# Optimization experiments

Measured on AMD Instinct MI355X. Metric: run time of the kernel, lower is better.

## Reference

```python
import jax, jax.numpy as jnp
import numpy as np

LEAK = 0.2
NUM_GRAPHS = 64


def _gat(h_in, src, dst, eh, W, att_src, att_dst, att_edge, lin_edge_W, bias, N):
    # PyG GATConv with edge_dim, concat=False (mean over heads)
    H, C = att_src.shape
    h = (h_in @ W).reshape(N, H, C)                      # [N,H,C]
    e = (eh @ lin_edge_W).reshape(-1, H, C)              # [Eaug,H,C]
    a_s = jnp.einsum('nhc,hc->nh', h, att_src)           # [N,H]
    a_d = jnp.einsum('nhc,hc->nh', h, att_dst)
    a_e = jnp.einsum('ehc,hc->eh', e, att_edge)          # [Eaug,H]
    score = jax.nn.leaky_relu(a_s[src] + a_d[dst] + a_e, LEAK)
    # scatter-softmax over incoming edges of each destination node
    m = jax.ops.segment_max(score, dst, num_segments=N)
    ex = jnp.exp(score - m[dst])
    den = jax.ops.segment_sum(ex, dst, num_segments=N)
    alpha = ex / den[dst]                                # [Eaug,H]
    out = jax.ops.segment_sum(alpha[:, :, None] * h[src], dst, num_segments=N)
    return out.mean(axis=1) + bias                       # concat=False -> head mean


def setup_inputs() -> dict:
    key = jax.random.key(0)
    ks = jax.random.split(key, 32)
    N, E, F, FE, HID, H, NT = 30000, 480000, 64, 16, 64, 4, 16
    Cin1 = F + HID
    s = 0.05
    d = {
        'x': jax.random.normal(ks[0], (N, F), jnp.float32),
        'edge_attr': jax.random.normal(ks[1], (E, FE), jnp.float32),
        'node_emb': jax.random.normal(ks[2], (NT, HID), jnp.float32) * s,
        'edge_W': jax.random.normal(ks[3], (FE, HID), jnp.float32) * s,
        'edge_b': jnp.zeros((HID,), jnp.float32),
        'W1': jax.random.normal(ks[4], (Cin1, H * HID), jnp.float32) * s,
        'as1': jax.random.normal(ks[5], (H, HID), jnp.float32) * s,
        'ad1': jax.random.normal(ks[6], (H, HID), jnp.float32) * s,
        'ae1': jax.random.normal(ks[7], (H, HID), jnp.float32) * s,
        'leW1': jax.random.normal(ks[8], (HID, H * HID), jnp.float32) * s,
        'b1': jnp.zeros((HID,), jnp.float32),
        'W2': jax.random.normal(ks[9], (HID, H * HID), jnp.float32) * s,
        'as2': jax.random.normal(ks[10], (H, HID), jnp.float32) * s,
        'ad2': jax.random.normal(ks[11], (H, HID), jnp.float32) * s,
        'ae2': jax.random.normal(ks[12], (H, HID), jnp.float32) * s,
        'leW2': jax.random.normal(ks[13], (HID, H * HID), jnp.float32) * s,
        'b2': jnp.zeros((HID,), jnp.float32),
        'sage_Wl': jax.random.normal(ks[14], (HID, HID), jnp.float32) * s,
        'sage_bl': jnp.zeros((HID,), jnp.float32),
        'sage_Wr': jax.random.normal(ks[15], (HID, HID), jnp.float32) * s,
        'lin1_W': jax.random.normal(ks[16], (HID, HID), jnp.float32) * s,
        'lin1_b': jnp.zeros((HID,), jnp.float32),
        'lin2_W': jax.random.normal(ks[17], (HID, HID), jnp.float32) * s,
        'lin2_b': jnp.zeros((HID,), jnp.float32),
        'tel_W': jax.random.normal(ks[18], (HID, 1), jnp.float32) * s,
        'tel_b': jnp.zeros((1,), jnp.float32),
        'comp_W': jax.random.normal(ks[19], (HID, 1), jnp.float32) * s,
        'comp_b': jnp.zeros((1,), jnp.float32),
        'pch_W': jax.random.normal(ks[20], (HID, 1), jnp.float32) * s,
        'pch_b': jnp.zeros((1,), jnp.float32),
        'edge_index': jax.random.randint(ks[21], (2, E), 0, N, jnp.int32),
        'batch': jnp.sort(jax.random.randint(ks[22], (N,), 0, NUM_GRAPHS, jnp.int32)),
        'node_type': jax.random.randint(ks[23], (N,), 0, NT, jnp.int32),
    }
    return d


def reference(x, edge_attr, node_emb, edge_W, edge_b,
              W1, as1, ad1, ae1, leW1, b1,
              W2, as2, ad2, ae2, leW2, b2,
              sage_Wl, sage_bl, sage_Wr,
              lin1_W, lin1_b, lin2_W, lin2_b,
              tel_W, tel_b, comp_W, comp_b, pch_W, pch_b,
              edge_index, batch, node_type):
    N = x.shape[0]
    src0, dst0 = edge_index[0], edge_index[1]

    h0 = jnp.concatenate([x, node_emb[node_type]], axis=-1)   # [N, F+HID]
    eh = edge_attr @ edge_W + edge_b                          # [E, HID]

    # GATConv default add_self_loops=True, fill_value='mean' on edge_attr
    loop = jnp.arange(N, dtype=src0.dtype)
    src = jnp.concatenate([src0, loop])
    dst = jnp.concatenate([dst0, loop])
    eh_aug = jnp.concatenate([eh, jnp.broadcast_to(eh.mean(axis=0), (N, eh.shape[1]))], axis=0)

    h1 = jax.nn.elu(_gat(h0, src, dst, eh_aug, W1, as1, ad1, ae1, leW1, b1, N))
    h2 = jax.nn.elu(_gat(h1, src, dst, eh_aug, W2, as2, ad2, ae2, leW2, b2, N))

    # SAGEConv: mean neighbor aggregation (src->dst) + root transform
    deg = jax.ops.segment_sum(jnp.ones_like(dst0, dtype=h2.dtype), dst0, num_segments=N)
    agg = jax.ops.segment_sum(h2[src0], dst0, num_segments=N) / jnp.clip(deg, 1.0)[:, None]
    h3 = jax.nn.elu(agg @ sage_Wl + sage_bl + h2 @ sage_Wr)

    # global mean pool per graph
    cnt = jax.ops.segment_sum(jnp.ones((N,), h3.dtype), batch, num_segments=NUM_GRAPHS)
    g = jax.ops.segment_sum(h3, batch, num_segments=NUM_GRAPHS) / jnp.clip(cnt, 1.0)[:, None]

    g = jax.nn.elu(g @ lin1_W + lin1_b)                       # dropout inactive (eval)
    g = g @ lin2_W + lin2_b
    return (g @ tel_W + tel_b, g @ comp_W + comp_b, g @ pch_W + pch_b)
```

## Files before the change

kernel.cpp:

```cpp
#include <hip/hip_runtime.h>
#include <hip/hip_fp16.h>
#include <math.h>

#define NN 30000
#define NE 480000
#define FEA 16
#define HID 64
#define NG 64
#define LEAKK 0.2f

#define S_AEL1   0
#define S_AEL2   4
#define S_KF1    16
#define S_C1     80
#define S_KF2    88
#define S_C2     152
#define S_MS1    160
#define S_MD1    672
#define S_MS2    1184
#define S_MD2    1440
#define S_EAS    1700

#define BT1H 0
#define BT1L 20480
#define BT2H 40960
#define BT2L 57344
#define BT3H 73728
#define BT3L 81920

typedef __attribute__((ext_vector_type(8))) short short8;
typedef __attribute__((ext_vector_type(4))) float f32x4;

__device__ __forceinline__ float eluf(float v) { return v > 0.f ? v : expm1f(v); }
__device__ __forceinline__ float leakyf(float v) { return v >= 0.f ? v : LEAKK * v; }
__device__ __forceinline__ void fma4(float4& a, float w, const float4& x) {
    a.x += w * x.x; a.y += w * x.y; a.z += w * x.z; a.w += w * x.w;
}
__device__ __forceinline__ unsigned bf16pack(float a, float b) {
    unsigned ua = __float_as_uint(a), ub = __float_as_uint(b);
    ua = (ua + 0x7FFFu + ((ua >> 16) & 1u)) >> 16;
    ub = (ub + 0x7FFFu + ((ub >> 16) & 1u)) >> 16;
    return ua | (ub << 16);
}
__device__ __forceinline__ unsigned short bf1(float v) {
    unsigned u = __float_as_uint(v);
    return (unsigned short)((u + 0x7FFFu + ((u >> 16) & 1u)) >> 16);
}
__device__ __forceinline__ float bf1tof(unsigned short h) {
    return __uint_as_float(((unsigned)h) << 16);
}
__device__ __forceinline__ uint2 bfpack4(float a, float b, float c, float d) {
    return make_uint2(bf16pack(a, b), bf16pack(c, d));
}
__device__ __forceinline__ float4 bf16x4(uint2 p) {
    float4 r;
    r.x = __uint_as_float(p.x << 16);
    r.y = __uint_as_float(p.x & 0xFFFF0000u);
    r.z = __uint_as_float(p.y << 16);
    r.w = __uint_as_float(p.y & 0xFFFF0000u);
    return r;
}
__device__ __forceinline__ unsigned h2pack(float a, float b) {
    __half2 h = __floats2half2_rn(a, b);
    return *(unsigned*)&h;
}
__device__ __forceinline__ float2 h2unpack(unsigned u) {
    __half2 h = *(__half2*)&u;
    return __half22float2(h);
}
__device__ __forceinline__ float4 h4tof(uint2 p) {
    float2 lo = h2unpack(p.x), hi = h2unpack(p.y);
    return make_float4(lo.x, lo.y, hi.x, hi.y);
}
__device__ __forceinline__ float4 escore4(float4 a, float4 b, float4 c) {
    float4 r;
    r.x = expf(leakyf(a.x + b.x + c.x));
    r.y = expf(leakyf(a.y + b.y + c.y));
    r.z = expf(leakyf(a.z + b.z + c.z));
    r.w = expf(leakyf(a.w + b.w + c.w));
    return r;
}


__global__ __launch_bounds__(256) void cm_prepw_kernel(
    const int* __restrict__ dst, const float* __restrict__ EA,
    int* __restrict__ cnt, int* __restrict__ rank,
    const float* __restrict__ W1, const float* __restrict__ W2,
    const float* __restrict__ Wl, const float* __restrict__ Wr,
    const float* __restrict__ emb,
    const float* __restrict__ leW1, const float* __restrict__ aew1,
    const float* __restrict__ leW2, const float* __restrict__ aew2,
    const float* __restrict__ edge_W, const float* __restrict__ edge_b,
    const float* __restrict__ as1, const float* __restrict__ ad1,
    const float* __restrict__ as2, const float* __restrict__ ad2,
    const int* __restrict__ batch,
    unsigned short* __restrict__ BT,
    float* __restrict__ S, int* __restrict__ goff) {
    int t = threadIdx.x, bx = blockIdx.x;
    if (bx < 176) {
        int i = bx * 256 + t;
        float v = 0.f;
        int dsti = -1;
        if (i < 16384) {
            int kk = i >> 6, c = i & 63;
            int h = kk >> 6, k = kk & 63;
            v = 0.25f * W1[k * 256 + h * 64 + c];
            dsti = BT1H + c * 320 + kk;
        } else if (i < 20480) {
            int j2 = i - 16384;
            int r2 = j2 >> 6, c = j2 & 63;
            int tau = r2 >> 2, h = r2 & 3;
            float acc = 0.f;
            for (int j = 0; j < 64; j++)
                acc += emb[tau * 64 + j] * W1[(64 + j) * 256 + h * 64 + c];
            v = 0.25f * acc;
            dsti = BT1H + c * 320 + 256 + r2;
        } else if (i < 36864) {
            int j = i - 20480;
            int kk = j >> 6, c = j & 63;
            int h = kk >> 6, k = kk & 63;
            v = 0.25f * W2[k * 256 + h * 64 + c];
            dsti = BT2H + c * 256 + kk;
        } else if (i < 45056) {
            int j = i - 36864;
            int k = j >> 6, c = j & 63;
            v = (k < 64) ? Wl[k * 64 + c] : Wr[(k - 64) * 64 + c];
            dsti = BT3H + c * 128 + k;
        }
        if (dsti >= 0) {
            unsigned short hi = bf1(v);
            unsigned short lo = bf1(v - bf1tof(hi));
            BT[dsti] = hi;
            BT[dsti + 20480 - ((dsti >= BT2H) ? ((dsti >= BT3H) ? 12288 : 4096) : 0)] = lo;
        }
        return;
    }
    if (bx < 178) {
        int i = (bx - 176) * 256 + t;
        int k = i >> 2, h = i & 3;
        float s = 0.f, d = 0.f;
        for (int c = 0; c < 64; c++) {
            float w = W1[k * 256 + h * 64 + c];
            s += w * as1[h * 64 + c];
            d += w * ad1[h * 64 + c];
        }
        S[S_MS1 + i] = s; S[S_MD1 + i] = d;
        return;
    }
    if (bx == 178) {
        int k = t >> 2, h = t & 3;
        float s = 0.f, d = 0.f;
        for (int c = 0; c < 64; c++) {
            float w = W2[k * 256 + h * 64 + c];
            s += w * as2[h * 64 + c];
            d += w * ad2[h * 64 + c];
        }
        S[S_MS2 + t] = s; S[S_MD2 + t] = d;
        return;
    }
    if (bx == 179) {
        __shared__ float M1s[256], M2s[256];
        {
            int k = t >> 2, h = t & 3;
            float m1 = 0.f, m2 = 0.f;
            for (int c = 0; c < 64; c++) {
                m1 += leW1[k * 256 + h * 64 + c] * aew1[h * 64 + c];
                m2 += leW2[k * 256 + h * 64 + c] * aew2[h * 64 + c];
            }
            M1s[t] = m1; M2s[t] = m2;
        }
        __syncthreads();
        if (t < 64) {
            int f = t >> 2, h = t & 3;
            float k1 = 0.f, k2 = 0.f;
            for (int k = 0; k < 64; k++) {
                k1 += edge_W[f * 64 + k] * M1s[k * 4 + h];
                k2 += edge_W[f * 64 + k] * M2s[k * 4 + h];
            }
            S[S_KF1 + t] = k1; S[S_KF2 + t] = k2;
        } else if (t < 68) {
            int h = t - 64;
            float c1 = 0.f, c2 = 0.f;
            for (int k = 0; k < 64; k++) {
                c1 += edge_b[k] * M1s[k * 4 + h];
                c2 += edge_b[k] * M2s[k * 4 + h];
            }
            S[S_C1 + h] = c1; S[S_C2 + h] = c2;
        }
        return;
    }
    if (bx == 180) {
        if (t > NG) return;
        int lo = 0, hi = NN;
        while (lo < hi) {
            int mid = (lo + hi) >> 1;
            if (batch[mid] < t) lo = mid + 1; else hi = mid;
        }
        goff[t] = lo;
        return;
    }
    if (bx < 245) {
        __shared__ float4 red4[16];
        int cb = bx - 181;
        int c4 = (t & 3) * 4;
        int r0 = cb * 64 + (t >> 2);
        float4 a0 = {0, 0, 0, 0}, a1 = a0, a2 = a0, a3 = a0;
        for (int r = r0; r < NE; r += 16384) {
            int r1 = r + 4096, r2 = r + 8192, r3 = r + 12288;
            float4 v0 = *(const float4*)(EA + (size_t)r * FEA + c4);
            float4 v1 = (r1 < NE) ? *(const float4*)(EA + (size_t)r1 * FEA + c4)
                                  : make_float4(0, 0, 0, 0);
            float4 v2 = (r2 < NE) ? *(const float4*)(EA + (size_t)r2 * FEA + c4)
                                  : make_float4(0, 0, 0, 0);
            float4 v3 = (r3 < NE) ? *(const float4*)(EA + (size_t)r3 * FEA + c4)
                                  : make_float4(0, 0, 0, 0);
            a0.x += v0.x; a0.y += v0.y; a0.z += v0.z; a0.w += v0.w;
            a1.x += v1.x; a1.y += v1.y; a1.z += v1.z; a1.w += v1.w;
            a2.x += v2.x; a2.y += v2.y; a2.z += v2.z; a2.w += v2.w;
            a3.x += v3.x; a3.y += v3.y; a3.z += v3.z; a3.w += v3.w;
        }
        float4 acc;
        acc.x = (a0.x + a1.x) + (a2.x + a3.x);
        acc.y = (a0.y + a1.y) + (a2.y + a3.y);
        acc.z = (a0.z + a1.z) + (a2.z + a3.z);
        acc.w = (a0.w + a1.w) + (a2.w + a3.w);
#pragma unroll
        for (int mask = 4; mask < 64; mask <<= 1) {
            acc.x += __shfl_xor(acc.x, mask, 64);
            acc.y += __shfl_xor(acc.y, mask, 64);
            acc.z += __shfl_xor(acc.z, mask, 64);
            acc.w += __shfl_xor(acc.w, mask, 64);
        }
        int lane = t & 63, wid = t >> 6;
        if (lane < 4) red4[wid * 4 + lane] = acc;
        __syncthreads();
        if (t < 4) {
            float4 a = red4[t], b = red4[4 + t], c = red4[8 + t], d = red4[12 + t];
            atomicAdd(&S[S_EAS + t * 4 + 0], a.x + b.x + c.x + d.x);
            atomicAdd(&S[S_EAS + t * 4 + 1], a.y + b.y + c.y + d.y);
            atomicAdd(&S[S_EAS + t * 4 + 2], a.z + b.z + c.z + d.z);
            atomicAdd(&S[S_EAS + t * 4 + 3], a.w + b.w + c.w + d.w);
        }
        return;
    }
    int e = (bx - 245) * 256 + t;
    if (e < NE) rank[e] = atomicAdd(&cnt[dst[e]], 1);
}

__global__ void scan_blocks_kernel(const int* __restrict__ cnt, int* __restrict__ eoff,
                                   int* __restrict__ bsum) {
    __shared__ int wsum[16];
    int t = threadIdx.x;
    int i = blockIdx.x * 1024 + t;
    int v = (i < NN) ? cnt[i] : 0;
    int lane = t & 63;
    int incl = v;
#pragma unroll
    for (int ofs = 1; ofs < 64; ofs <<= 1) {
        int u = __shfl_up(incl, ofs, 64);
        if (lane >= ofs) incl += u;
    }
    int wid = t >> 6;
    if (lane == 63) wsum[wid] = incl;
    __syncthreads();
    if (t < 16) {
        int s = wsum[t];
#pragma unroll
        for (int ofs = 1; ofs < 16; ofs <<= 1) {
            int u = __shfl_up(s, ofs, 64);
            if (t >= ofs) s += u;
        }
        wsum[t] = s;
    }
    __syncthreads();
    int excl = incl - v + (wid > 0 ? wsum[wid - 1] : 0);
    if (i < NN) eoff[i] = excl;
    if (t == 1023) bsum[blockIdx.x] = excl + v;
}

__global__ __launch_bounds__(256) void scanadd_attn_kernel(
    const int* __restrict__ bsum, int* __restrict__ eoff,
    const float* __restrict__ x, const float* __restrict__ node_emb,
    const int* __restrict__ node_type, float* __restrict__ S,
    float* __restrict__ as_, float* __restrict__ ad_, unsigned* __restrict__ xb) {
    __shared__ float xt[64 * 132];
    __shared__ float ms[512], md[512];
    __shared__ int ntS[64];
    int t = threadIdx.x;
    if (blockIdx.x < 118) {
        int j = blockIdx.x >> 2;
        int pref = 0;
        for (int u = 0; u < j; u++) pref += bsum[u];
        int i = blockIdx.x * 256 + t;
        if (i < NN) eoff[i] += pref;
        if (i == 0) eoff[NN] = NE;
        return;
    }
    if (blockIdx.x == 118) {
        if (t < 8) {
            int h = t & 3;
            const float* KF = (t < 4) ? (S + S_KF1) : (S + S_KF2);
            const float* C  = (t < 4) ? (S + S_C1)  : (S + S_C2);
            float acc = (float)NE * C[h];
            for (int f = 0; f < 16; f++) acc += S[S_EAS + f] * KF[f * 4 + h];
            S[((t < 4) ? S_AEL1 : S_AEL2) + h] = acc;
        }
        return;
    }
    int n0 = (blockIdx.x - 119) * 64;
    if (t < 64) {
        int n = n0 + t;
        ntS[t] = (n < NN) ? node_type[n] : 0;
    }
    for (int i = t; i < 512; i += 256) { ms[i] = S[S_MS1 + i]; md[i] = S[S_MD1 + i]; }
    __syncthreads();
    for (int i = t; i < 1024; i += 256) {
        int r = i >> 4, c4 = (i & 15) * 4;
        int n = n0 + r;
        float4 f = {0, 0, 0, 0};
        if (n < NN) f = *(const float4*)(x + (size_t)n * 64 + c4);
        *(float4*)&xt[r * 132 + c4] = f;
    }
    for (int i = t; i < 1024; i += 256) {
        int r = i >> 4, c4 = (i & 15) * 4;
        int n = n0 + r;
        float4 f = {0, 0, 0, 0};
        if (n < NN) f = *(const float4*)(node_emb + (size_t)ntS[r] * 64 + c4);
        *(float4*)&xt[r * 132 + 64 + c4] = f;
    }
    __syncthreads();
    for (int i = t; i < 2048; i += 256) {
        int r = i >> 5, u = i & 31;
        int n = n0 + r;
        if (n < NN)
            xb[(size_t)n * 32 + u] = bf16pack(xt[r * 132 + 2 * u], xt[r * 132 + 2 * u + 1]);
    }
    int r = t >> 2, h = t & 3;
    float s = 0.f, d = 0.f;
#pragma unroll 8
    for (int k = 0; k < 128; k++) {
        float xv = xt[r * 132 + k];
        s += xv * ms[k * 4 + h];
        d += xv * md[k * 4 + h];
    }
    int n = n0 + r;
    if (n < NN) { as_[n * 4 + h] = s; ad_[n * 4 + h] = d; }
}

__global__ __launch_bounds__(256) void scatter_proj_kernel(
    const int* __restrict__ src, const int* __restrict__ dst,
    const float* __restrict__ EA, const float* __restrict__ S,
    const float* __restrict__ as_, const float* __restrict__ ad_,
    const int* __restrict__ node_type,
    const int* __restrict__ eoff, const int* __restrict__ rank,
    uint4* __restrict__ recs) {
    __shared__ float KF1s[64], KF2s[64], Cs[8];
    int t = threadIdx.x;
    if (t < 64) { KF1s[t] = S[S_KF1 + t]; KF2s[t] = S[S_KF2 + t]; }
    else if (t < 72) { int q = t - 64; Cs[q] = (q < 4) ? S[S_C1 + q] : S[S_C2 + q - 4]; }
    __syncthreads();
    int e0 = blockIdx.x * 512 + t;
#pragma unroll
    for (int u = 0; u < 2; u++) {
        int e = e0 + u * 256;
        if (e < NE) {
            int s = src[e], d = dst[e];
            float a1[4], a2[4];
#pragma unroll
            for (int h = 0; h < 4; h++) { a1[h] = Cs[h]; a2[h] = Cs[4 + h]; }
            const float4* EA4 = (const float4*)(EA + (size_t)e * FEA);
#pragma unroll
            for (int q = 0; q < 4; q++) {
                float4 v = EA4[q];
                float vv[4] = {v.x, v.y, v.z, v.w};
#pragma unroll
                for (int j = 0; j < 4; j++) {
                    int f = q * 4 + j;
#pragma unroll
                    for (int h = 0; h < 4; h++) {
                        a1[h] += vv[j] * KF1s[f * 4 + h];
                        a2[h] += vv[j] * KF2s[f * 4 + h];
                    }
                }
            }
            int pos = eoff[d] + rank[e];
            float4 asv = ((const float4*)as_)[s];
            float4 adv = ((const float4*)ad_)[d];
            float4 w1 = escore4(asv, adv, make_float4(a1[0], a1[1], a1[2], a1[3]));
            uint4 lo = make_uint4(h2pack(w1.x, w1.y), h2pack(w1.z, w1.w),
                                  h2pack(a2[0], a2[1]), h2pack(a2[2], a2[3]));
            uint4 hi = make_uint4((unsigned)(s | (node_type[s] << 16)), (unsigned)d, 0u, 0u);
            recs[2 * pos] = lo;
            recs[2 * pos + 1] = hi;
        }
    }
}

__global__ __launch_bounds__(256) void score2_kernel(
    uint4* __restrict__ recs,
    const float* __restrict__ as_, const float* __restrict__ ad_,
    int* __restrict__ sepc) {
    int p = blockIdx.x * 256 + threadIdx.x;
    uint2 a2h = ((const uint2*)recs)[4 * p + 1];
    int2 sd = ((const int2*)recs)[4 * p + 2];
    int s = sd.x & 0xFFFF;
    float4 w2 = escore4(((const float4*)as_)[s], ((const float4*)ad_)[sd.y], h4tof(a2h));
    ((uint2*)recs)[4 * p + 1] = make_uint2(h2pack(w2.x, w2.y), h2pack(w2.z, w2.w));
    sepc[p] = sd.x;
}

__global__ __launch_bounds__(256) void agg_gat1_kernel(
    const int* __restrict__ eoff, const uint4* __restrict__ recs,
    const unsigned* __restrict__ xb,
    const int* __restrict__ node_type,
    const float* __restrict__ as_, const float* __restrict__ ad_,
    const float* __restrict__ S, uint2* __restrict__ aggb) {
    int n = blockIdx.x * 4 + (threadIdx.x >> 6);
    if (n >= NN) return;
    int lane = threadIdx.x & 63;
    int sub = lane >> 4, ch = lane & 15;
    const uint2* Xb = (const uint2*)xb;
    const int* RI = (const int*)recs;
    const uint2* RW = (const uint2*)recs;
    float4 asn = ((const float4*)as_)[n];
    float4 adn = ((const float4*)ad_)[n];
    float4 a0 = {0, 0, 0, 0}, a1 = a0, a2 = a0, a3 = a0, dn = a0, tw = a0;
    int b = eoff[n], e_end = eoff[n + 1];
    int nE = e_end - b;
    int i = sub;
    for (; i + 4 < nE; i += 8) {
        int p0 = b + i, p1 = p0 + 4;
        int q0 = RI[8 * p0 + 4], q1 = RI[8 * p1 + 4];
        int s0 = q0 & 0xFFFF, t0 = q0 >> 16;
        int s1 = q1 & 0xFFFF, t1 = q1 >> 16;
        float4 w0 = h4tof(RW[4 * p0]), w1 = h4tof(RW[4 * p1]);
        float4 x0 = bf16x4(Xb[(size_t)s0 * 16 + ch]);
        float4 x1 = bf16x4(Xb[(size_t)s1 * 16 + ch]);
        fma4(a0, w0.x, x0); fma4(a1, w0.y, x0); fma4(a2, w0.z, x0); fma4(a3, w0.w, x0);
        fma4(a0, w1.x, x1); fma4(a1, w1.y, x1); fma4(a2, w1.z, x1); fma4(a3, w1.w, x1);
        dn.x += w0.x + w1.x; dn.y += w0.y + w1.y;
        dn.z += w0.z + w1.z; dn.w += w0.w + w1.w;
        if (ch == t0) { tw.x += w0.x; tw.y += w0.y; tw.z += w0.z; tw.w += w0.w; }
        if (ch == t1) { tw.x += w1.x; tw.y += w1.y; tw.z += w1.z; tw.w += w1.w; }
    }
    for (; i < nE; i += 4) {
        int p0 = b + i;
        int q0 = RI[8 * p0 + 4];
        int s0 = q0 & 0xFFFF, t0 = q0 >> 16;
        float4 w0 = h4tof(RW[4 * p0]);
        float4 x0 = bf16x4(Xb[(size_t)s0 * 16 + ch]);
        fma4(a0, w0.x, x0); fma4(a1, w0.y, x0); fma4(a2, w0.z, x0); fma4(a3, w0.w, x0);
        dn.x += w0.x; dn.y += w0.y; dn.z += w0.z; dn.w += w0.w;
        if (ch == t0) { tw.x += w0.x; tw.y += w0.y; tw.z += w0.z; tw.w += w0.w; }
    }
    if (sub == 0) {
        const float inv = 1.f / (float)NE;
        float e0 = expf(leakyf(asn.x + adn.x + S[S_AEL1 + 0] * inv));
        float e1 = expf(leakyf(asn.y + adn.y + S[S_AEL1 + 1] * inv));
        float e2 = expf(leakyf(asn.z + adn.z + S[S_AEL1 + 2] * inv));
        float e3 = expf(leakyf(asn.w + adn.w + S[S_AEL1 + 3] * inv));
        float4 xs = bf16x4(Xb[(size_t)n * 16 + ch]);
        fma4(a0, e0, xs); fma4(a1, e1, xs); fma4(a2, e2, xs); fma4(a3, e3, xs);
        dn.x += e0; dn.y += e1; dn.z += e2; dn.w += e3;
        int tn = node_type[n];
        if (ch == tn) { tw.x += e0; tw.y += e1; tw.z += e2; tw.w += e3; }
    }
#pragma unroll
    for (int mask = 16; mask < 64; mask <<= 1) {
        a0.x += __shfl_xor(a0.x, mask, 64); a0.y += __shfl_xor(a0.y, mask, 64);
        a0.z += __shfl_xor(a0.z, mask, 64); a0.w += __shfl_xor(a0.w, mask, 64);
        a1.x += __shfl_xor(a1.x, mask, 64); a1.y += __shfl_xor(a1.y, mask, 64);
        a1.z += __shfl_xor(a1.z, mask, 64); a1.w += __shfl_xor(a1.w, mask, 64);
        a2.x += __shfl_xor(a2.x, mask, 64); a2.y += __shfl_xor(a2.y, mask, 64);
        a2.z += __shfl_xor(a2.z, mask, 64); a2.w += __shfl_xor(a2.w, mask, 64);
        a3.x += __shfl_xor(a3.x, mask, 64); a3.y += __shfl_xor(a3.y, mask, 64);
        a3.z += __shfl_xor(a3.z, mask, 64); a3.w += __shfl_xor(a3.w, mask, 64);
        dn.x += __shfl_xor(dn.x, mask, 64); dn.y += __shfl_xor(dn.y, mask, 64);
        dn.z += __shfl_xor(dn.z, mask, 64); dn.w += __shfl_xor(dn.w, mask, 64);
        tw.x += __shfl_xor(tw.x, mask, 64); tw.y += __shfl_xor(tw.y, mask, 64);
        tw.z += __shfl_xor(tw.z, mask, 64); tw.w += __shfl_xor(tw.w, mask, 64);
    }
    if (sub == 0) {
        float i0 = 1.f / dn.x, i1 = 1.f / dn.y, i2 = 1.f / dn.z, i3 = 1.f / dn.w;
        uint2* A2 = aggb + (size_t)n * 80;
        A2[ch]      = bfpack4(a0.x * i0, a0.y * i0, a0.z * i0, a0.w * i0);
        A2[16 + ch] = bfpack4(a1.x * i1, a1.y * i1, a1.z * i1, a1.w * i1);
        A2[32 + ch] = bfpack4(a2.x * i2, a2.y * i2, a2.z * i2, a2.w * i2);
        A2[48 + ch] = bfpack4(a3.x * i3, a3.y * i3, a3.z * i3, a3.w * i3);
        A2[64 + ch] = bfpack4(tw.x * i0, tw.y * i1, tw.z * i2, tw.w * i3);
    }
}

__global__ __launch_bounds__(256) void agg_gat2_kernel(
    const int* __restrict__ eoff, const uint4* __restrict__ recs,
    const unsigned* __restrict__ h1b,
    const float* __restrict__ as_, const float* __restrict__ ad_,
    const float* __restrict__ S, uint2* __restrict__ aggb) {
    int n = blockIdx.x * 4 + (threadIdx.x >> 6);
    if (n >= NN) return;
    int lane = threadIdx.x & 63;
    int sub = lane >> 4, ch = lane & 15;
    const uint2* Xb = (const uint2*)h1b;
    const int* RI = (const int*)recs;
    const uint2* RW = (const uint2*)recs;
    float4 asn = ((const float4*)as_)[n];
    float4 adn = ((const float4*)ad_)[n];
    float4 a0 = {0, 0, 0, 0}, a1 = a0, a2 = a0, a3 = a0, dn = a0;
    int b = eoff[n], e = eoff[n + 1];
    int nE = e - b;
    int i = sub;
    for (; i + 4 < nE; i += 8) {
        int p0 = b + i, p1 = p0 + 4;
        int s0 = RI[8 * p0 + 4] & 0xFFFF, s1 = RI[8 * p1 + 4] & 0xFFFF;
        float4 w0 = h4tof(RW[4 * p0 + 1]), w1 = h4tof(RW[4 * p1 + 1]);
        float4 x0 = bf16x4(Xb[(size_t)s0 * 16 + ch]);
        float4 x1 = bf16x4(Xb[(size_t)s1 * 16 + ch]);
        fma4(a0, w0.x, x0); fma4(a1, w0.y, x0); fma4(a2, w0.z, x0); fma4(a3, w0.w, x0);
        fma4(a0, w1.x, x1); fma4(a1, w1.y, x1); fma4(a2, w1.z, x1); fma4(a3, w1.w, x1);
        dn.x += w0.x + w1.x; dn.y += w0.y + w1.y;
        dn.z += w0.z + w1.z; dn.w += w0.w + w1.w;
    }
    for (; i < nE; i += 4) {
        int p0 = b + i;
        int s0 = RI[8 * p0 + 4] & 0xFFFF;
        float4 w0 = h4tof(RW[4 * p0 + 1]);
        float4 x0 = bf16x4(Xb[(size_t)s0 * 16 + ch]);
        fma4(a0, w0.x, x0); fma4(a1, w0.y, x0); fma4(a2, w0.z, x0); fma4(a3, w0.w, x0);
        dn.x += w0.x; dn.y += w0.y; dn.z += w0.z; dn.w += w0.w;
    }
    if (sub == 0) {
        const float inv = 1.f / (float)NE;
        float e0 = expf(leakyf(asn.x + adn.x + S[S_AEL2 + 0] * inv));
        float e1 = expf(leakyf(asn.y + adn.y + S[S_AEL2 + 1] * inv));
        float e2 = expf(leakyf(asn.z + adn.z + S[S_AEL2 + 2] * inv));
        float e3 = expf(leakyf(asn.w + adn.w + S[S_AEL2 + 3] * inv));
        float4 xs = bf16x4(Xb[(size_t)n * 16 + ch]);
        fma4(a0, e0, xs); fma4(a1, e1, xs); fma4(a2, e2, xs); fma4(a3, e3, xs);
        dn.x += e0; dn.y += e1; dn.z += e2; dn.w += e3;
    }
#pragma unroll
    for (int mask = 16; mask < 64; mask <<= 1) {
        a0.x += __shfl_xor(a0.x, mask, 64); a0.y += __shfl_xor(a0.y, mask, 64);
        a0.z += __shfl_xor(a0.z, mask, 64); a0.w += __shfl_xor(a0.w, mask, 64);
        a1.x += __shfl_xor(a1.x, mask, 64); a1.y += __shfl_xor(a1.y, mask, 64);
        a1.z += __shfl_xor(a1.z, mask, 64); a1.w += __shfl_xor(a1.w, mask, 64);
        a2.x += __shfl_xor(a2.x, mask, 64); a2.y += __shfl_xor(a2.y, mask, 64);
        a2.z += __shfl_xor(a2.z, mask, 64); a2.w += __shfl_xor(a2.w, mask, 64);
        a3.x += __shfl_xor(a3.x, mask, 64); a3.y += __shfl_xor(a3.y, mask, 64);
        a3.z += __shfl_xor(a3.z, mask, 64); a3.w += __shfl_xor(a3.w, mask, 64);
        dn.x += __shfl_xor(dn.x, mask, 64); dn.y += __shfl_xor(dn.y, mask, 64);
        dn.z += __shfl_xor(dn.z, mask, 64); dn.w += __shfl_xor(dn.w, mask, 64);
    }
    if (sub == 0) {
        float i0 = 1.f / dn.x, i1 = 1.f / dn.y, i2 = 1.f / dn.z, i3 = 1.f / dn.w;
        uint2* A2 = aggb + (size_t)n * 64;
        A2[ch]      = bfpack4(a0.x * i0, a0.y * i0, a0.z * i0, a0.w * i0);
        A2[16 + ch] = bfpack4(a1.x * i1, a1.y * i1, a1.z * i1, a1.w * i1);
        A2[32 + ch] = bfpack4(a2.x * i2, a2.y * i2, a2.z * i2, a2.w * i2);
        A2[48 + ch] = bfpack4(a3.x * i3, a3.y * i3, a3.z * i3, a3.w * i3);
    }
}

template <int K, bool DOATT>
__global__ __launch_bounds__(256) void gemm_mfma_kernel(
    const unsigned* __restrict__ A, const unsigned short* __restrict__ bth,
    const unsigned short* __restrict__ btl,
    const float* __restrict__ bias, float* __restrict__ out,
    unsigned short* __restrict__ out16,
    const float* __restrict__ ms_g, const float* __restrict__ md_g,
    float* __restrict__ as_, float* __restrict__ ad_) {
    int t = threadIdx.x;
    int w = t >> 6, l = t & 63;
    int lr = l & 15, lg = l >> 4;
    int m0 = blockIdx.x * 64 + w * 16;
    int am = m0 + lr;
    bool av = am < NN;
    const short8* Arow = (const short8*)A + (size_t)am * (K / 8);
    short8 zz = {0, 0, 0, 0, 0, 0, 0, 0};
    f32x4 acc[4];
#pragma unroll
    for (int ct = 0; ct < 4; ct++) acc[ct] = (f32x4){0.f, 0.f, 0.f, 0.f};
#pragma unroll
    for (int k0 = 0; k0 < K; k0 += 32) {
        short8 a = av ? Arow[(k0 >> 3) + lg] : zz;
#pragma unroll
        for (int ct = 0; ct < 4; ct++) {
            int bo = (ct * 16 + lr) * K + k0 + lg * 8;
            short8 bh = *(const short8*)(bth + bo);
            short8 bl = *(const short8*)(btl + bo);
            acc[ct] = __builtin_amdgcn_mfma_f32_16x16x32_bf16(a, bh, acc[ct], 0, 0, 0);
            acc[ct] = __builtin_amdgcn_mfma_f32_16x16x32_bf16(a, bl, acc[ct], 0, 0, 0);
        }
    }
    f32x4 ps[4], pd[4];
    if (DOATT) {
#pragma unroll
        for (int r = 0; r < 4; r++) {
            ps[r] = (f32x4){0.f, 0.f, 0.f, 0.f};
            pd[r] = (f32x4){0.f, 0.f, 0.f, 0.f};
        }
    }
#pragma unroll
    for (int ct = 0; ct < 4; ct++) {
        int col = ct * 16 + lr;
        float bv = bias[col];
        f32x4 ms4, md4;
        if (DOATT) {
            ms4 = ((const f32x4*)ms_g)[col];
            md4 = ((const f32x4*)md_g)[col];
        }
#pragma unroll
        for (int r = 0; r < 4; r++) {
            int m = m0 + lg * 4 + r;
            float o = eluf(acc[ct][r] + bv);
            if (m < NN) {
                if (out) out[(size_t)m * 64 + col] = o;
                if (out16) out16[(size_t)m * 64 + col] = bf1(o);
            }
            if (DOATT) { ps[r] += o * ms4; pd[r] += o * md4; }
        }
    }
    if (DOATT) {
#pragma unroll
        for (int mk = 1; mk < 16; mk <<= 1)
#pragma unroll
            for (int r = 0; r < 4; r++) {
                ps[r][0] += __shfl_xor(ps[r][0], mk, 64);
                ps[r][1] += __shfl_xor(ps[r][1], mk, 64);
                ps[r][2] += __shfl_xor(ps[r][2], mk, 64);
                ps[r][3] += __shfl_xor(ps[r][3], mk, 64);
                pd[r][0] += __shfl_xor(pd[r][0], mk, 64);
                pd[r][1] += __shfl_xor(pd[r][1], mk, 64);
                pd[r][2] += __shfl_xor(pd[r][2], mk, 64);
                pd[r][3] += __shfl_xor(pd[r][3], mk, 64);
            }
        if (lr == 0) {
#pragma unroll
            for (int r = 0; r < 4; r++) {
                int m = m0 + lg * 4 + r;
                if (m < NN) {
                    *(f32x4*)(as_ + (size_t)m * 4) = ps[r];
                    *(f32x4*)(ad_ + (size_t)m * 4) = pd[r];
                }
            }
        }
    }
}

__global__ __launch_bounds__(256) void sage_agg3_kernel(
    const unsigned* __restrict__ h2b,
    const int* __restrict__ eoff, const int* __restrict__ sepc,
    uint2* __restrict__ AB) {
    int n = blockIdx.x * 16 + (threadIdx.x >> 4);
    if (n >= NN) return;
    int l = threadIdx.x & 15;
    const uint2* Hb = (const uint2*)h2b;
    float ax = 0.f, ay = 0.f, az = 0.f, aw = 0.f;
    int b = eoff[n], e_end = eoff[n + 1];
    int idx = b;
    int stop = b + ((e_end - b) & ~7);
    if (idx < stop) {
        int sreg[8];
#pragma unroll
        for (int u = 0; u < 8; u++) sreg[u] = sepc[idx + u] & 0xFFFF;
        idx += 8;
        while (true) {
            int sn[8];
            bool more = idx < stop;
            if (more) {
#pragma unroll
                for (int u = 0; u < 8; u++) sn[u] = sepc[idx + u] & 0xFFFF;
            }
#pragma unroll
            for (int u = 0; u < 8; u++) {
                float4 v = bf16x4(Hb[(size_t)sreg[u] * 16 + l]);
                ax += v.x; ay += v.y; az += v.z; aw += v.w;
            }
            if (!more) break;
#pragma unroll
            for (int u = 0; u < 8; u++) sreg[u] = sn[u];
            idx += 8;
        }
    }
    for (; idx < e_end; idx++) {
        float4 v0 = bf16x4(Hb[(size_t)(sepc[idx] & 0xFFFF) * 16 + l]);
        ax += v0.x; ay += v0.y; az += v0.z; aw += v0.w;
    }
    float dg = (float)(e_end - b);
    if (dg < 1.f) dg = 1.f;
    float inv = 1.f / dg;
    AB[(size_t)n * 32 + l] = bfpack4(ax * inv, ay * inv, az * inv, aw * inv);
    AB[(size_t)n * 32 + 16 + l] = Hb[(size_t)n * 16 + l];
}

__global__ __launch_bounds__(256) void pool_mlp_kernel(
    const float* __restrict__ h3, const int* __restrict__ goff,
    const float* __restrict__ lin1W, const float* __restrict__ lin1b,
    const float* __restrict__ lin2W, const float* __restrict__ lin2b,
    const float* __restrict__ telW, const float* __restrict__ telb,
    const float* __restrict__ compW, const float* __restrict__ compb,
    const float* __restrict__ pchW, const float* __restrict__ pchb,
    float* __restrict__ out) {
    __shared__ float red[256];
    __shared__ float g[64], G1[64], G2[64];
    int gi = blockIdx.x, t = threadIdx.x;
    int c = t & 63, li = t >> 6;
    int b = goff[gi], e = goff[gi + 1];
    float sum = 0.f;
    for (int r = b + li; r < e; r += 4) sum += h3[(size_t)r * HID + c];
    red[t] = sum;
    __syncthreads();
    if (t < 64) {
        float v = red[t] + red[t + 64] + red[t + 128] + red[t + 192];
        float cntf = (float)(e - b);
        if (cntf < 1.f) cntf = 1.f;
        g[t] = v / cntf;
    }
    __syncthreads();
    {
        float part = 0.f;
#pragma unroll
        for (int k = li * 16; k < li * 16 + 16; k++) part += g[k] * lin1W[k * 64 + c];
        red[t] = part;
        __syncthreads();
        if (t < 64)
            G1[c] = eluf(red[c] + red[c + 64] + red[c + 128] + red[c + 192] + lin1b[c]);
        __syncthreads();
    }
    {
        float part = 0.f;
#pragma unroll
        for (int k = li * 16; k < li * 16 + 16; k++) part += G1[k] * lin2W[k * 64 + c];
        red[t] = part;
        __syncthreads();
        if (t < 64)
            G2[c] = red[c] + red[c + 64] + red[c + 128] + red[c + 192] + lin2b[c];
        __syncthreads();
    }
    if (t < 192) {
        int h = t >> 6, k = t & 63;
        const float* W = (h == 0) ? telW : ((h == 1) ? compW : pchW);
        red[t] = G2[k] * W[k];
    }
    __syncthreads();
    if (t < 3) {
        float acc = 0.f;
        for (int k = 0; k < 64; k++) acc += red[t * 64 + k];
        float bb = (t == 0) ? telb[0] : ((t == 1) ? compb[0] : pchb[0]);
        out[t * 64 + gi] = acc + bb;
    }
}

extern "C" void kernel_launch(void* const* d_in, const int* in_sizes, int n_in,
                              void* d_out, int out_size, void* d_ws, size_t ws_size,
                              hipStream_t stream) {
    const float* x        = (const float*)d_in[0];
    const float* EA       = (const float*)d_in[1];
    const float* node_emb = (const float*)d_in[2];
    const float* edge_W   = (const float*)d_in[3];
    const float* edge_b   = (const float*)d_in[4];
    const float* W1       = (const float*)d_in[5];
    const float* as1      = (const float*)d_in[6];
    const float* ad1      = (const float*)d_in[7];
    const float* ae1      = (const float*)d_in[8];
    const float* leW1     = (const float*)d_in[9];
    const float* b1       = (const float*)d_in[10];
    const float* W2       = (const float*)d_in[11];
    const float* as2      = (const float*)d_in[12];
    const float* ad2      = (const float*)d_in[13];
    const float* ae2      = (const float*)d_in[14];
    const float* leW2     = (const float*)d_in[15];
    const float* b2       = (const float*)d_in[16];
    const float* sage_Wl  = (const float*)d_in[17];
    const float* sage_bl  = (const float*)d_in[18];
    const float* sage_Wr  = (const float*)d_in[19];
    const float* lin1_W   = (const float*)d_in[20];
    const float* lin1_b   = (const float*)d_in[21];
    const float* lin2_W   = (const float*)d_in[22];
    const float* lin2_b   = (const float*)d_in[23];
    const float* tel_W    = (const float*)d_in[24];
    const float* tel_b    = (const float*)d_in[25];
    const float* comp_W   = (const float*)d_in[26];
    const float* comp_b   = (const float*)d_in[27];
    const float* pch_W    = (const float*)d_in[28];
    const float* pch_b    = (const float*)d_in[29];
    const int* edge_index = (const int*)d_in[30];
    const int* batch      = (const int*)d_in[31];
    const int* node_type  = (const int*)d_in[32];
    float* outp = (float*)d_out;

    const int* srcp = edge_index;
    const int* dstp = edge_index + NE;

    float* wf = (float*)d_ws;
    constexpr size_t OFF_H3    = 0;
    constexpr size_t OFF_AGG   = OFF_H3 + (size_t)NN * 64;
    constexpr size_t OFF_REC   = OFF_AGG + (size_t)NN * 512;
    constexpr size_t OFF_AS    = OFF_REC + (size_t)NE * 8;
    constexpr size_t OFF_AD    = OFF_AS + (size_t)NN * 4;
    constexpr size_t OFF_SMALL = OFF_AD + (size_t)NN * 4;
    constexpr size_t OFF_BT    = OFF_SMALL + 4096;
    constexpr size_t OFF_XB    = OFF_BT + 45056;
    constexpr size_t OFF_H1B   = OFF_XB + (size_t)NN * 32;
    constexpr size_t OFF_H2B   = OFF_H1B + (size_t)NN * 32;
    constexpr size_t F_TOTAL   = OFF_H2B + (size_t)NN * 32;

    int* wi   = (int*)(wf + F_TOTAL);
    int* cnt  = wi;
    int* rank = wi + NN;
    int* eoff = rank + NE;
    int* sepc = eoff + (NN + 2);
    int* goff = sepc + NE;
    int* bsum = goff + (NG + 1);

    float* h3    = wf + OFF_H3;
    float* aggb  = wf + OFF_AGG;
    uint4* recs  = (uint4*)(wf + OFF_REC);
    float* as_   = wf + OFF_AS;
    float* ad_   = wf + OFF_AD;
    float* S     = wf + OFF_SMALL;
    unsigned short* BT = (unsigned short*)(wf + OFF_BT);
    unsigned* xb  = (unsigned*)(wf + OFF_XB);
    unsigned short* h1b = (unsigned short*)(wf + OFF_H1B);
    unsigned short* h2b = (unsigned short*)(wf + OFF_H2B);

    hipMemsetAsync(S + S_EAS, 0, 16 * sizeof(float), stream);
    hipMemsetAsync(cnt, 0, NN * sizeof(int), stream);

    cm_prepw_kernel<<<245 + (NE + 255) / 256, 256, 0, stream>>>(
        dstp, EA, cnt, rank, W1, W2, sage_Wl, sage_Wr, node_emb,
        leW1, ae1, leW2, ae2, edge_W, edge_b, as1, ad1, as2, ad2, batch,
        BT, S, goff);

    scan_blocks_kernel<<<(NN + 1023) / 1024, 1024, 0, stream>>>(cnt, eoff, bsum);
    scanadd_attn_kernel<<<119 + (NN + 63) / 64, 256, 0, stream>>>(
        bsum, eoff, x, node_emb, node_type, S, as_, ad_, xb);

    scatter_proj_kernel<<<(NE + 511) / 512, 256, 0, stream>>>(
        srcp, dstp, EA, S, as_, ad_, node_type, eoff, rank, recs);

    agg_gat1_kernel<<<(NN + 3) / 4, 256, 0, stream>>>(
        eoff, recs, xb, node_type, as_, ad_, S, (uint2*)aggb);
    gemm_mfma_kernel<320, true><<<(NN + 63) / 64, 256, 0, stream>>>(
        (const unsigned*)aggb, BT + BT1H, BT + BT1L, b1, nullptr, h1b,
        S + S_MS2, S + S_MD2, as_, ad_);

    score2_kernel<<<NE / 256, 256, 0, stream>>>(recs, as_, ad_, sepc);
    agg_gat2_kernel<<<(NN + 3) / 4, 256, 0, stream>>>(
        eoff, recs, (const unsigned*)h1b, as_, ad_, S, (uint2*)aggb);
    gemm_mfma_kernel<256, false><<<(NN + 63) / 64, 256, 0, stream>>>(
        (const unsigned*)aggb, BT + BT2H, BT + BT2L, b2, nullptr, h2b,
        nullptr, nullptr, nullptr, nullptr);

    sage_agg3_kernel<<<(NN + 15) / 16, 256, 0, stream>>>(
        (const unsigned*)h2b, eoff, sepc, (uint2*)aggb);
    gemm_mfma_kernel<128, false><<<(NN + 63) / 64, 256, 0, stream>>>(
        (const unsigned*)aggb, BT + BT3H, BT + BT3L, sage_bl, h3, nullptr,
        nullptr, nullptr, nullptr, nullptr);

    pool_mlp_kernel<<<NG, 256, 0, stream>>>(h3, goff, lin1_W, lin1_b, lin2_W, lin2_b,
                                            tel_W, tel_b, comp_W, comp_b, pch_W, pch_b, outp);
}
```

Before: 365.3 us.

## Replace per-edge rank array with atomic cursor slots in CSR scatter

Drops the per-edge rank array. Edge placement now uses a per-node cursor: the scan seeds it with the CSR offset and the scatter kernel takes each edge's slot with an atomicAdd. Count and cursor arrays are padded to a stride of 8 ints, which puts each node's counter in its own 32-byte sector and is meant to cut atomic contention. The counting pass also handles 4 edges per thread. In exchange, edge order within each destination segment becomes nondeterministic, which can change floating-point summation order, and the scatter kernel now issues a second round of atomics.

After: 375.6 us. 1.03x slower.

```diff
diff --git a/kernel.cpp b/kernel.cpp
--- a/kernel.cpp
+++ b/kernel.cpp
@@ -84,7 +84,7 @@
 
 __global__ __launch_bounds__(256) void cm_prepw_kernel(
     const int* __restrict__ dst, const float* __restrict__ EA,
-    int* __restrict__ cnt, int* __restrict__ rank,
+    int* __restrict__ cnt,
     const float* __restrict__ W1, const float* __restrict__ W2,
     const float* __restrict__ Wl, const float* __restrict__ Wr,
     const float* __restrict__ emb,
@@ -243,8 +243,12 @@
         }
         return;
     }
-    int e = (bx - 245) * 256 + t;
-    if (e < NE) rank[e] = atomicAdd(&cnt[dst[e]], 1);
+    int base = (bx - 245) * 1024;
+#pragma unroll
+    for (int u = 0; u < 4; u++) {
+        int e = base + u * 256 + t;
+        if (e < NE) atomicAdd(&cnt[dst[e] * 8], 1);
+    }
 }
 
 __global__ void scan_blocks_kernel(const int* __restrict__ cnt, int* __restrict__ eoff,
@@ -252,7 +256,7 @@
     __shared__ int wsum[16];
     int t = threadIdx.x;
     int i = blockIdx.x * 1024 + t;
-    int v = (i < NN) ? cnt[i] : 0;
+    int v = (i < NN) ? cnt[i * 8] : 0;
     int lane = t & 63;
     int incl = v;
 #pragma unroll
@@ -279,7 +283,7 @@
 }
 
 __global__ __launch_bounds__(256) void scanadd_attn_kernel(
-    const int* __restrict__ bsum, int* __restrict__ eoff,
+    const int* __restrict__ bsum, int* __restrict__ eoff, int* __restrict__ ecur,
     const float* __restrict__ x, const float* __restrict__ node_emb,
     const int* __restrict__ node_type, float* __restrict__ S,
     float* __restrict__ as_, float* __restrict__ ad_, unsigned* __restrict__ xb) {
@@ -292,7 +296,11 @@
         int pref = 0;
         for (int u = 0; u < j; u++) pref += bsum[u];
         int i = blockIdx.x * 256 + t;
-        if (i < NN) eoff[i] += pref;
+        if (i < NN) {
+            int v = eoff[i] + pref;
+            eoff[i] = v;
+            ecur[i * 8] = v;
+        }
         if (i == 0) eoff[NN] = NE;
         return;
     }
@@ -352,7 +360,7 @@
     const float* __restrict__ EA, const float* __restrict__ S,
     const float* __restrict__ as_, const float* __restrict__ ad_,
     const int* __restrict__ node_type,
-    const int* __restrict__ eoff, const int* __restrict__ rank,
+    int* __restrict__ ecur,
     uint4* __restrict__ recs) {
     __shared__ float KF1s[64], KF2s[64], Cs[8];
     int t = threadIdx.x;
@@ -365,6 +373,7 @@
         int e = e0 + u * 256;
         if (e < NE) {
             int s = src[e], d = dst[e];
+            int pos = atomicAdd(&ecur[d * 8], 1);
             float a1[4], a2[4];
 #pragma unroll
             for (int h = 0; h < 4; h++) { a1[h] = Cs[h]; a2[h] = Cs[4 + h]; }
@@ -383,7 +392,6 @@
                     }
                 }
             }
-            int pos = eoff[d] + rank[e];
             float4 asv = ((const float4*)as_)[s];
             float4 adv = ((const float4*)ad_)[d];
             float4 w1 = escore4(asv, adv, make_float4(a1[0], a1[1], a1[2], a1[3]));
@@ -807,8 +815,8 @@
 
     int* wi   = (int*)(wf + F_TOTAL);
     int* cnt  = wi;
-    int* rank = wi + NN;
-    int* eoff = rank + NE;
+    int* ecur = wi + NN * 8;
+    int* eoff = ecur + NN * 8;
     int* sepc = eoff + (NN + 2);
     int* goff = sepc + NE;
     int* bsum = goff + (NG + 1);
@@ -825,19 +833,19 @@
     unsigned short* h2b = (unsigned short*)(wf + OFF_H2B);
 
     hipMemsetAsync(S + S_EAS, 0, 16 * sizeof(float), stream);
-    hipMemsetAsync(cnt, 0, NN * sizeof(int), stream);
-
-    cm_prepw_kernel<<<245 + (NE + 255) / 256, 256, 0, stream>>>(
-        dstp, EA, cnt, rank, W1, W2, sage_Wl, sage_Wr, node_emb,
+    hipMemsetAsync(cnt, 0, NN * 8 * sizeof(int), stream);
+
+    cm_prepw_kernel<<<245 + (NE + 1023) / 1024, 256, 0, stream>>>(
+        dstp, EA, cnt, W1, W2, sage_Wl, sage_Wr, node_emb,
         leW1, ae1, leW2, ae2, edge_W, edge_b, as1, ad1, as2, ad2, batch,
         BT, S, goff);
 
     scan_blocks_kernel<<<(NN + 1023) / 1024, 1024, 0, stream>>>(cnt, eoff, bsum);
     scanadd_attn_kernel<<<119 + (NN + 63) / 64, 256, 0, stream>>>(
-        bsum, eoff, x, node_emb, node_type, S, as_, ad_, xb);
+        bsum, eoff, ecur, x, node_emb, node_type, S, as_, ad_, xb);
 
     scatter_proj_kernel<<<(NE + 511) / 512, 256, 0, stream>>>(
-        srcp, dstp, EA, S, as_, ad_, node_type, eoff, rank, recs);
+        srcp, dstp, EA, S, as_, ad_, node_type, ecur, recs);
 
     agg_gat1_kernel<<<(NN + 3) / 4, 256, 0, stream>>>(
         eoff, recs, xb, node_type, as_, ad_, S, (uint2*)aggb);
```
